# Kernel tuning notes

Measured on AMD Instinct MI355X. Metric: run time of the kernel, lower is better.

The kernel has to match this reference:

```python
import jax, jax.numpy as jnp
import numpy as np
import math

DIM = 2048
NUM_HEADS = 32
HEAD_DIM = DIM // NUM_HEADS  # 64; HEAD_DIM//2 == NUM_HEADS (required by original rope broadcasting)
SEQ_LEN = 2048
BATCH = 2
ROPE_BASE = 10000.0


def apply_rope(inputs, positions):
    # Faithful to original: positions is [L]; sinusoid broadcasts to [1, L, H/2, 1]
    # and then multiplies [B, L, N, H/2] -- the original code relies on N == H/2.
    head_dim = inputs.shape[-1]
    fraction = 2.0 * jnp.arange(head_dim // 2, dtype=inputs.dtype) / head_dim
    timescale = ROPE_BASE ** fraction                      # [H/2]
    sinusoid = positions[:, None] / timescale[None, None, :]  # [1, L, H/2]
    sinusoid = sinusoid[..., None]                         # [1, L, H/2, 1]
    sin = jnp.sin(sinusoid)
    cos = jnp.cos(sinusoid)
    first, second = jnp.split(inputs, 2, axis=-1)          # each [B, L, N, H/2]
    return jnp.concatenate([first * cos - second * sin,
                            second * cos + first * sin], axis=-1)


def setup_inputs() -> dict:
    key = jax.random.key(0)
    ks = jax.random.split(key, 9)
    s = 0.02
    inp = {
        'x': jax.random.normal(ks[0], (BATCH, SEQ_LEN, DIM), dtype=jnp.float32),
        'wq_w': jax.random.normal(ks[1], (DIM, DIM), dtype=jnp.float32) * s,
        'wq_b': jnp.zeros((DIM,), dtype=jnp.float32),
        'wk_w': jax.random.normal(ks[2], (DIM, DIM), dtype=jnp.float32) * s,
        'wk_b': jnp.zeros((DIM,), dtype=jnp.float32),
        'wv_w': jax.random.normal(ks[3], (DIM, DIM), dtype=jnp.float32) * s,
        'wv_b': jnp.zeros((DIM,), dtype=jnp.float32),
        'wo_w': jax.random.normal(ks[4], (DIM, DIM), dtype=jnp.float32) * s,
        'wo_b': jnp.zeros((DIM,), dtype=jnp.float32),
    }
    return inp


def reference(x, wq_w, wq_b, wk_w, wk_b, wv_w, wv_b, wo_w, wo_b):
    B, L, _ = x.shape
    N, H = NUM_HEADS, HEAD_DIM
    q = (x @ wq_w.T + wq_b).reshape(B, L, N, H)
    k = (x @ wk_w.T + wk_b).reshape(B, L, N, H)
    v = (x @ wv_w.T + wv_b).reshape(B, L, N, H)
    positions = jnp.arange(L, dtype=x.dtype)
    q = apply_rope(q, positions)
    k = apply_rope(k, positions)
    # [B, N, L, H]
    q = q.transpose(0, 2, 1, 3)
    k = k.transpose(0, 2, 1, 3)
    v = v.transpose(0, 2, 1, 3)
    scale = math.sqrt(H)
    scores = jnp.einsum('bnqh,bnkh->bnqk', q, k) / scale   # [B, N, L, L]
    causal = jnp.tril(jnp.ones((L, L), dtype=bool))
    scores = jnp.where(causal[None, None], scores, -jnp.inf)
    attn = jax.nn.softmax(scores, axis=-1)
    context = jnp.einsum('bnqk,bnkh->bnqh', attn, v)        # [B, N, L, H]
    context = context.transpose(0, 2, 1, 3).reshape(B, L, DIM)
    return context @ wo_w.T + wo_b
```

## Files before the change

kernel.cpp:

```cpp
#include <hip/hip_runtime.h>
#include <stdint.h>

#define D_MODEL 2048
#define SEQLEN  2048

typedef float f32x4  __attribute__((ext_vector_type(4)));
typedef float f32x16 __attribute__((ext_vector_type(16)));
typedef int   i32x4  __attribute__((ext_vector_type(4)));
typedef short s16x4  __attribute__((ext_vector_type(4)));
typedef __bf16 bf16x8 __attribute__((ext_vector_type(8)));

__device__ __forceinline__ unsigned short f2bf(float f) {
  union { float f; uint32_t u; } x; x.f = f;
  uint32_t r = (x.u + 0x7FFFu + ((x.u >> 16) & 1u)) >> 16;
  return (unsigned short)r;
}

__device__ __forceinline__ uint32_t cvtpk(float lo, float hi) {
  uint32_t r;
  asm("v_cvt_pk_bf16_f32 %0, %1, %2" : "=v"(r) : "v"(lo), "v"(hi));
  return r;
}

__device__ __forceinline__ bf16x8 as_bf16x8(i32x4 v) {
  union { i32x4 i; bf16x8 b; } u; u.i = v; return u.b;
}

#define MFMA16(acc, a, b) \
  acc = __builtin_amdgcn_mfma_f32_16x16x32_bf16(as_bf16x8(a), as_bf16x8(b), acc, 0, 0, 0)
#define MFMA32(acc, a, b) \
  acc = __builtin_amdgcn_mfma_f32_32x32x16_bf16(as_bf16x8(a), as_bf16x8(b), acc, 0, 0, 0)

__device__ __forceinline__ void gload16(const void* g, void* lds) {
  __builtin_amdgcn_global_load_lds(
      (const __attribute__((address_space(1))) unsigned int*)(uintptr_t)g,
      (__attribute__((address_space(3))) unsigned int*)(uint32_t)(uintptr_t)lds,
      16, 0, 0);
}

__global__ void cvt_all_k(const float* __restrict__ x,
                          const float* __restrict__ w0, const float* __restrict__ w1,
                          const float* __restrict__ w2, const float* __restrict__ w3,
                          unsigned short* __restrict__ xo,
                          unsigned short* __restrict__ o0, unsigned short* __restrict__ o1,
                          unsigned short* __restrict__ o2, unsigned short* __restrict__ o3) {
  const int i = blockIdx.x * 256 + threadIdx.x;
  const float* src; unsigned short* dst; int off;
  if (i < 2097152) { src = x; dst = xo; off = i; }
  else {
    const int j = i - 2097152, seg = j >> 20;
    off = j & 1048575;
    src = seg == 0 ? w0 : seg == 1 ? w1 : seg == 2 ? w2 : w3;
    dst = seg == 0 ? o0 : seg == 1 ? o1 : seg == 2 ? o2 : o3;
  }
  f32x4 v = *(const f32x4*)&src[(size_t)off * 4];
  s16x4 o;
#pragma unroll
  for (int j = 0; j < 4; ++j) o[j] = (short)f2bf(v[j]);
  *(s16x4*)&dst[(size_t)off * 4] = o;
}

template <bool ROPE, bool F32OUT>
__global__ __launch_bounds__(512) void gemm1(
    const unsigned short* __restrict__ A,
    const unsigned short* __restrict__ W,
    const float* __restrict__ bias,
    unsigned short* __restrict__ Ob,
    float* __restrict__ Of) {
  constexpr int PLANE_E = 384 * 32;
  __shared__ alignas(16) unsigned short L[4 * PLANE_E];

  const int t = threadIdx.x;
  const int w = t >> 6, l = t & 63;
  const int wm = w >> 1, wn = w & 1;
  const int band = l >> 4, ln = l & 15;

  const int m0 = blockIdx.y * 256;
  const int nloc = blockIdx.x * 128;

  auto stage1 = [&](int p, int ktile, int b, int i) {
    unsigned short* dst = L + (b * 2 + p) * PLANE_E;
    const int idx = w * 3 + i;
    const int row = idx * 16 + (l >> 2);
    const int gblk = (l & 3) ^ ((row >> 1) & 3);
    const int kcol = ktile * 64 + p * 32;
    const unsigned short* src =
        (idx < 16) ? &A[(size_t)(m0 + row) * D_MODEL + kcol + gblk * 8]
                   : &W[(size_t)(nloc + row - 256) * D_MODEL + kcol + gblk * 8];
    gload16(src, dst + idx * 512);
  };
  auto ld = [&](const unsigned short* pl, int r) {
    return *(const i32x4*)&pl[r * 32 + (((band ^ (r >> 1)) & 3) << 3)];
  };

  f32x4 acc[4][4] = {};

#pragma unroll
  for (int i = 0; i < 3; ++i) stage1(0, 0, 0, i);
#pragma unroll
  for (int i = 0; i < 3; ++i) stage1(1, 0, 0, i);
  asm volatile("s_waitcnt vmcnt(3)" ::: "memory");
  __builtin_amdgcn_s_barrier();

  for (int kt = 0; kt < 32; ++kt) {
    const int rb = kt & 1;
    const int ktn = (kt + 1) & 31;
#pragma unroll
    for (int kh = 0; kh < 2; ++kh) {
      const unsigned short* pl = L + (rb * 2 + kh) * PLANE_E;
      i32x4 bv[4], av[2];
#pragma unroll
      for (int nf = 0; nf < 4; ++nf) bv[nf] = ld(pl, 256 + wn * 64 + nf * 16 + ln);
#pragma unroll
      for (int mf = 0; mf < 2; ++mf) av[mf] = ld(pl, wm * 64 + mf * 16 + ln);
      stage1(kh, ktn, rb ^ 1, 0);
      stage1(kh, ktn, rb ^ 1, 1);
      __builtin_amdgcn_s_barrier();
      asm volatile("s_waitcnt lgkmcnt(0)" ::: "memory");
      __builtin_amdgcn_sched_barrier(0);
      __builtin_amdgcn_s_setprio(1);
#pragma unroll
      for (int mf = 0; mf < 2; ++mf)
#pragma unroll
        for (int nf = 0; nf < 4; ++nf) MFMA16(acc[mf][nf], av[mf], bv[nf]);
      __builtin_amdgcn_s_setprio(0);
      __builtin_amdgcn_s_barrier();
#pragma unroll
      for (int mf = 0; mf < 2; ++mf) av[mf] = ld(pl, wm * 64 + (2 + mf) * 16 + ln);
      stage1(kh, ktn, rb ^ 1, 2);
      __builtin_amdgcn_s_barrier();
      asm volatile("s_waitcnt lgkmcnt(0)" ::: "memory");
      __builtin_amdgcn_sched_barrier(0);
      __builtin_amdgcn_s_setprio(1);
#pragma unroll
      for (int mf = 0; mf < 2; ++mf)
#pragma unroll
        for (int nf = 0; nf < 4; ++nf) MFMA16(acc[2 + mf][nf], av[mf], bv[nf]);
      __builtin_amdgcn_s_setprio(0);
      asm volatile("s_waitcnt vmcnt(3)" ::: "memory");
      __builtin_amdgcn_s_barrier();
    }
  }
  asm volatile("s_waitcnt vmcnt(0)" ::: "memory");

  float bb[4];
#pragma unroll
  for (int nf = 0; nf < 4; ++nf) bb[nf] = bias[nloc + wn * 64 + nf * 16 + ln];

  const int head = (nloc + wn * 64) >> 6;
  const float ts = powf(10000.0f, (float)head * (1.0f / 32.0f));
#pragma unroll
  for (int am = 0; am < 4; ++am) {
#pragma unroll
    for (int r = 0; r < 4; ++r) {
      const int row = m0 + wm * 64 + am * 16 + band * 4 + r;
      float vals[4];
#pragma unroll
      for (int nf = 0; nf < 4; ++nf) vals[nf] = acc[am][nf][r] + bb[nf];
      if constexpr (ROPE) {
        const float pos = (float)(row & (SEQLEN - 1));
        float sv, cv;
        __sincosf(pos / ts, &sv, &cv);
#pragma unroll
        for (int pp = 0; pp < 2; ++pp) {
          const float f0 = vals[pp], s0 = vals[pp + 2];
          vals[pp]     = f0 * cv - s0 * sv;
          vals[pp + 2] = s0 * cv + f0 * sv;
        }
      }
#pragma unroll
      for (int nf = 0; nf < 4; ++nf) {
        const size_t oi = (size_t)row * D_MODEL + nloc + wn * 64 + nf * 16 + ln;
        if constexpr (F32OUT) Of[oi] = vals[nf];
        else                  Ob[oi] = f2bf(vals[nf]);
      }
    }
  }
}

__global__ __launch_bounds__(256) void attn_fwd(
    const unsigned short* __restrict__ Q, const unsigned short* __restrict__ K,
    const unsigned short* __restrict__ V, unsigned short* __restrict__ O) {
  __shared__ alignas(16) unsigned short Ks[2][64 * 64];
  __shared__ alignas(16) unsigned short Vt[2][64 * 80];

  const int t = threadIdx.x;
  const int w = t >> 6, l = t & 63;
  const int l31 = l & 31, t5 = l >> 5;
  const int bx = blockIdx.x, head = blockIdx.y, b = blockIdx.z;
  const int h0 = head * 64;
  const size_t rb = (size_t)b * SEQLEN;

  const int vg = t & 7, vrow = t >> 3;
  const int kdr = l >> 3, kdb = l & 7;

  for (int pi = 0; pi < 2; ++pi) {
    const int qt = pi ? (15 - bx) : bx;
    const int q0 = qt * 128;
    const int qg = q0 + w * 32 + l31;

    i32x4 qf[4];
#pragma unroll
    for (int hk = 0; hk < 4; ++hk)
      qf[hk] = *(const i32x4*)&Q[(rb + qg) * D_MODEL + h0 + hk * 16 + t5 * 8];

    f32x16 oacc[2] = {};
    float lsum = 0.f;
    const int nkt = qt * 2 + 2;

    {
#pragma unroll
      for (int i = 0; i < 2; ++i) {
        const int drow = (i * 4 + w) * 8 + kdr;
        const int sblk = kdb ^ (drow & 7);
        gload16(&K[(rb + drow) * D_MODEL + h0 + sblk * 8], &Ks[0][(i * 4 + w) * 512]);
      }
      i32x4 vv[2];
#pragma unroll
      for (int i = 0; i < 2; ++i)
        vv[i] = *(const i32x4*)&V[(rb + i * 32 + vrow) * D_MODEL + h0 + vg * 8];
      asm volatile("s_waitcnt vmcnt(0)" ::: "memory");
#pragma unroll
      for (int i = 0; i < 2; ++i) {
        const int r = i * 32 + vrow, c8 = vg * 8;
        union { i32x4 v; unsigned short s[8]; } u; u.v = vv[i];
#pragma unroll
        for (int j = 0; j < 8; ++j) Vt[0][(c8 + j) * 80 + (r ^ c8)] = u.s[j];
      }
    }
    __syncthreads();

    for (int kt = 0; kt < nkt; ++kt) {
      const int cur = kt & 1, nxt = cur ^ 1;
      const int k0 = kt * 64;
      const bool more = (kt + 1 < nkt);

      i32x4 vv[2];
      if (more) {
        const int k1 = k0 + 64;
#pragma unroll
        for (int i = 0; i < 2; ++i) {
          const int drow = (i * 4 + w) * 8 + kdr;
          const int sblk = kdb ^ (drow & 7);
          gload16(&K[(rb + k1 + drow) * D_MODEL + h0 + sblk * 8],
                  &Ks[nxt][(i * 4 + w) * 512]);
        }
#pragma unroll
        for (int i = 0; i < 2; ++i)
          vv[i] = *(const i32x4*)&V[(rb + k1 + i * 32 + vrow) * D_MODEL + h0 + vg * 8];
      }

      f32x16 sacc[2] = {};
#pragma unroll
      for (int kvf = 0; kvf < 2; ++kvf) {
        const int krow = kvf * 32 + l31;
#pragma unroll
        for (int hk = 0; hk < 4; ++hk) {
          i32x4 a = *(const i32x4*)&Ks[cur][krow * 64 + ((2 * hk + t5) ^ (krow & 7)) * 8];
          MFMA32(sacc[kvf], a, qf[hk]);
        }
      }

      const bool needmask = (k0 + 64 > q0 + w * 32);
      uint32_t W[2][4][2];
#pragma unroll
      for (int kvf = 0; kvf < 2; ++kvf)
#pragma unroll
        for (int g = 0; g < 4; ++g)
#pragma unroll
          for (int p = 0; p < 2; ++p) {
            float pv[2];
#pragma unroll
            for (int e = 0; e < 2; ++e) {
              const int reg = 4 * g + 2 * p + e;
              const int kvl = kvf * 32 + 8 * g + 4 * t5 + 2 * p + e;
              pv[e] = __expf(sacc[kvf][reg] * 0.125f);
              if (needmask && (k0 + kvl > qg)) pv[e] = 0.f;
              lsum += pv[e];
            }
            W[kvf][g][p] = cvtpk(pv[0], pv[1]);
          }

#pragma unroll
      for (int ks = 0; ks < 4; ++ks) {
        const int kvf = ks >> 1;
        const int gA = 2 * (ks & 1), gB = gA + 1;
        uint32_t a0 = W[kvf][gA][0], b0 = W[kvf][gB][0];
        uint32_t a1 = W[kvf][gA][1], b1 = W[kvf][gB][1];
        asm("v_permlane32_swap_b32 %0, %1" : "+v"(a0), "+v"(b0));
        asm("v_permlane32_swap_b32 %0, %1" : "+v"(a1), "+v"(b1));
        i32x4 pf;
        pf[0] = (int)a0; pf[1] = (int)a1; pf[2] = (int)b0; pf[3] = (int)b1;
#pragma unroll
        for (int hf = 0; hf < 2; ++hf) {
          const int h = hf * 32 + l31;
          i32x4 vb = *(const i32x4*)&Vt[cur][h * 80 + ((ks * 16 + t5 * 8) ^ ((h >> 3) * 8))];
          MFMA32(oacc[hf], pf, vb);
        }
      }

      if (more) {
        asm volatile("s_waitcnt vmcnt(0)" ::: "memory");
#pragma unroll
        for (int i = 0; i < 2; ++i) {
          const int r = i * 32 + vrow, c8 = vg * 8;
          union { i32x4 v; unsigned short s[8]; } u; u.v = vv[i];
#pragma unroll
          for (int j = 0; j < 8; ++j) Vt[nxt][(c8 + j) * 80 + (r ^ c8)] = u.s[j];
        }
      }
      __syncthreads();
    }

    lsum += __shfl_xor(lsum, 32);
    const float inv = 1.0f / lsum;

#pragma unroll
    for (int g2 = 0; g2 < 4; ++g2)
#pragma unroll
      for (int rr = 0; rr < 4; ++rr) {
        const int rowl = rr + 8 * g2 + 4 * t5;
        const float invr = __shfl(inv, (l & 32) + rowl);
        const size_t gr = rb + q0 + w * 32 + rowl;
#pragma unroll
        for (int hf = 0; hf < 2; ++hf)
          O[gr * D_MODEL + h0 + hf * 32 + l31] = f2bf(oacc[hf][4 * g2 + rr] * invr);
      }
  }
}

extern "C" void kernel_launch(void* const* d_in, const int* in_sizes, int n_in,
                              void* d_out, int out_size, void* d_ws, size_t ws_size,
                              hipStream_t stream) {
  const float* x    = (const float*)d_in[0];
  const float* wq_w = (const float*)d_in[1];
  const float* wq_b = (const float*)d_in[2];
  const float* wk_w = (const float*)d_in[3];
  const float* wk_b = (const float*)d_in[4];
  const float* wv_w = (const float*)d_in[5];
  const float* wv_b = (const float*)d_in[6];
  const float* wo_w = (const float*)d_in[7];
  const float* wo_b = (const float*)d_in[8];
  float* out = (float*)d_out;

  unsigned short* ws  = (unsigned short*)d_ws;
  unsigned short* xb  = ws;
  unsigned short* wqb = xb  + 8388608;
  unsigned short* wkb = wqb + 4194304;
  unsigned short* wvb = wkb + 4194304;
  unsigned short* wob = wvb + 4194304;
  unsigned short* qb  = wob + 4194304;
  unsigned short* kb  = qb  + 8388608;
  unsigned short* vb  = kb  + 8388608;
  unsigned short* cb  = xb;

  cvt_all_k<<<24576, 256, 0, stream>>>(x, wq_w, wk_w, wv_w, wo_w,
                                       xb, wqb, wkb, wvb, wob);

  dim3 g(16, 16);
  gemm1<true,  false><<<g, 512, 0, stream>>>(xb, wqb, wq_b, qb, nullptr);
  gemm1<true,  false><<<g, 512, 0, stream>>>(xb, wkb, wk_b, kb, nullptr);
  gemm1<false, false><<<g, 512, 0, stream>>>(xb, wvb, wv_b, vb, nullptr);

  attn_fwd<<<dim3(8, 32, 2), 256, 0, stream>>>(qb, kb, vb, cb);

  gemm1<false, true><<<g, 512, 0, stream>>>(cb, wob, wo_b, nullptr, out);
}
```

Baseline: 264.7 us.

## Remap GEMM block order, specialize mask path, add setprio and unroll attention loop

The GEMM remaps its block index so consecutive blocks share weight column tiles, which is meant to improve L2 reuse. In attention, the loop is unrolled by two with compile-time buffer indices, the first MFMA starts from a zero constant instead of a zeroed accumulator, and the masked and unmasked softmax paths are split so full tiles skip the compare. s_setprio raises wave priority around the MFMA sections to interleave matrix and exp work across waves. These changes add code size and register pressure, and unrolling by two relies on nkt being even, which holds because nkt = 2*qt+2.

```diff
diff --git a/kernel.cpp b/kernel.cpp
--- a/kernel.cpp
+++ b/kernel.cpp
@@ -75,8 +75,9 @@
   const int wm = w >> 1, wn = w & 1;
   const int band = l >> 4, ln = l & 15;
 
-  const int m0 = blockIdx.y * 256;
-  const int nloc = blockIdx.x * 128;
+  const int fid = blockIdx.y * 16 + blockIdx.x;
+  const int m0 = ((fid & 7) + 8 * ((fid >> 3) & 1)) * 256;
+  const int nloc = (fid >> 4) * 128;
 
   auto stage1 = [&](int p, int ktile, int b, int i) {
     unsigned short* dst = L + (b * 2 + p) * PLANE_E;
@@ -194,6 +195,8 @@
   const int vg = t & 7, vrow = t >> 3;
   const int kdr = l >> 3, kdb = l & 7;
 
+  const f32x16 fzero = {};
+
   for (int pi = 0; pi < 2; ++pi) {
     const int qt = pi ? (15 - bx) : bx;
     const int q0 = qt * 128;
@@ -230,8 +233,8 @@
     }
     __syncthreads();
 
-    for (int kt = 0; kt < nkt; ++kt) {
-      const int cur = kt & 1, nxt = cur ^ 1;
+    auto tile = [&](const int kt, const int cur) {
+      const int nxt = cur ^ 1;
       const int k0 = kt * 64;
       const bool more = (kt + 1 < nkt);
 
@@ -250,37 +253,62 @@
           vv[i] = *(const i32x4*)&V[(rb + k1 + i * 32 + vrow) * D_MODEL + h0 + vg * 8];
       }
 
-      f32x16 sacc[2] = {};
+      f32x16 sacc[2];
+      __builtin_amdgcn_s_setprio(1);
 #pragma unroll
       for (int kvf = 0; kvf < 2; ++kvf) {
         const int krow = kvf * 32 + l31;
-#pragma unroll
-        for (int hk = 0; hk < 4; ++hk) {
-          i32x4 a = *(const i32x4*)&Ks[cur][krow * 64 + ((2 * hk + t5) ^ (krow & 7)) * 8];
+        i32x4 a0 = *(const i32x4*)&Ks[cur][krow * 64 + ((t5 ^ (krow & 7)) << 3)];
+        sacc[kvf] = __builtin_amdgcn_mfma_f32_32x32x16_bf16(
+            as_bf16x8(a0), as_bf16x8(qf[0]), fzero, 0, 0, 0);
+#pragma unroll
+        for (int hk = 1; hk < 4; ++hk) {
+          i32x4 a = *(const i32x4*)&Ks[cur][krow * 64 + (((2 * hk + t5) ^ (krow & 7)) << 3)];
           MFMA32(sacc[kvf], a, qf[hk]);
         }
       }
+      __builtin_amdgcn_s_setprio(0);
 
       const bool needmask = (k0 + 64 > q0 + w * 32);
       uint32_t W[2][4][2];
-#pragma unroll
-      for (int kvf = 0; kvf < 2; ++kvf)
-#pragma unroll
-        for (int g = 0; g < 4; ++g)
-#pragma unroll
-          for (int p = 0; p < 2; ++p) {
-            float pv[2];
-#pragma unroll
-            for (int e = 0; e < 2; ++e) {
-              const int reg = 4 * g + 2 * p + e;
-              const int kvl = kvf * 32 + 8 * g + 4 * t5 + 2 * p + e;
-              pv[e] = __expf(sacc[kvf][reg] * 0.125f);
-              if (needmask && (k0 + kvl > qg)) pv[e] = 0.f;
-              lsum += pv[e];
+      if (needmask) {
+        const int qgk = qg - k0;
+#pragma unroll
+        for (int kvf = 0; kvf < 2; ++kvf)
+#pragma unroll
+          for (int g = 0; g < 4; ++g)
+#pragma unroll
+            for (int p = 0; p < 2; ++p) {
+              float pv[2];
+#pragma unroll
+              for (int e = 0; e < 2; ++e) {
+                const int reg = 4 * g + 2 * p + e;
+                const int kvl = kvf * 32 + 8 * g + 4 * t5 + 2 * p + e;
+                pv[e] = __expf(sacc[kvf][reg] * 0.125f);
+                if (kvl > qgk) pv[e] = 0.f;
+                lsum += pv[e];
+              }
+              W[kvf][g][p] = cvtpk(pv[0], pv[1]);
             }
-            W[kvf][g][p] = cvtpk(pv[0], pv[1]);
-          }
-
+      } else {
+#pragma unroll
+        for (int kvf = 0; kvf < 2; ++kvf)
+#pragma unroll
+          for (int g = 0; g < 4; ++g)
+#pragma unroll
+            for (int p = 0; p < 2; ++p) {
+              float pv[2];
+#pragma unroll
+              for (int e = 0; e < 2; ++e) {
+                const int reg = 4 * g + 2 * p + e;
+                pv[e] = __expf(sacc[kvf][reg] * 0.125f);
+                lsum += pv[e];
+              }
+              W[kvf][g][p] = cvtpk(pv[0], pv[1]);
+            }
+      }
+
+      __builtin_amdgcn_s_setprio(1);
 #pragma unroll
       for (int ks = 0; ks < 4; ++ks) {
         const int kvf = ks >> 1;
@@ -298,6 +326,7 @@
           MFMA32(oacc[hf], pf, vb);
         }
       }
+      __builtin_amdgcn_s_setprio(0);
 
       if (more) {
         asm volatile("s_waitcnt vmcnt(0)" ::: "memory");
@@ -310,6 +339,11 @@
         }
       }
       __syncthreads();
+    };
+
+    for (int kt = 0; kt < nkt; kt += 2) {
+      tile(kt, 0);
+      tile(kt + 1, 1);
     }
 
     lsum += __shfl_xor(lsum, 32);
```

Measured after the change: 272.3 us. 2.9% more time.
